# Optimization experiments

Hardware: AMD Instinct MI355X
Metric: run time of the kernel (lower is better)

Reference implementation:

```python
import jax, jax.numpy as jnp
import numpy as np

H = 16
D_MODEL = 1024
D_K = D_MODEL // H
B, S = 4, 2048


def setup_inputs() -> dict:
    key = jax.random.key(0)
    ks = jax.random.split(key, 12)
    scale = 1.0 / np.sqrt(D_MODEL)
    inp = {
        "q": jax.random.normal(ks[0], (B, S, D_MODEL), dtype=jnp.float32),
        "k": jax.random.normal(ks[1], (B, S, D_MODEL), dtype=jnp.float32),
        "v": jax.random.normal(ks[2], (B, S, D_MODEL), dtype=jnp.float32),
        # torch nn.Linear weights: shape (out, in), y = x @ W.T + b
        "Wq": jax.random.uniform(ks[3], (D_MODEL, D_MODEL), minval=-scale, maxval=scale),
        "bq": jax.random.uniform(ks[4], (D_MODEL,), minval=-scale, maxval=scale),
        "Wk": jax.random.uniform(ks[5], (D_MODEL, D_MODEL), minval=-scale, maxval=scale),
        "bk": jax.random.uniform(ks[6], (D_MODEL,), minval=-scale, maxval=scale),
        "Wv": jax.random.uniform(ks[7], (D_MODEL, D_MODEL), minval=-scale, maxval=scale),
        "bv": jax.random.uniform(ks[8], (D_MODEL,), minval=-scale, maxval=scale),
        "Wo": jax.random.uniform(ks[9], (D_MODEL, D_MODEL), minval=-scale, maxval=scale),
        "bo": jax.random.uniform(ks[10], (D_MODEL,), minval=-scale, maxval=scale),
        "ln_g": jnp.ones((D_MODEL,), dtype=jnp.float32),
        "ln_b": jnp.zeros((D_MODEL,), dtype=jnp.float32),
    }
    return inp


def _layernorm(x, g, b, eps=1e-5):
    mu = jnp.mean(x, axis=-1, keepdims=True)
    var = jnp.var(x, axis=-1, keepdims=True)
    return (x - mu) * jax.lax.rsqrt(var + eps) * g + b


def reference(q, k, v, Wq, bq, Wk, bk, Wv, bv, Wo, bo, ln_g, ln_b):
    nb = q.shape[0]
    # projections, split heads -> (B, H, S, d_k)
    def proj(x, W, b):
        y = x @ W.T + b
        return y.reshape(nb, -1, H, D_K).transpose(0, 2, 1, 3)

    Q = proj(q, Wq, bq)
    K = proj(k, Wk, bk)
    V = proj(v, Wv, bv)

    scores = jnp.einsum("bhqd,bhkd->bhqk", Q, K) / jnp.sqrt(jnp.float32(D_K))
    p_attn = jax.nn.softmax(scores, axis=-1)
    x = jnp.einsum("bhqk,bhkd->bhqd", p_attn, V)
    x = x.transpose(0, 2, 1, 3).reshape(nb, -1, H * D_K)
    out = _layernorm(x @ Wo.T + bo + q, ln_g, ln_b)
    return out
```

## Files before the change

### kernel.cpp

```cpp
#include <hip/hip_runtime.h>

#define DM 1024
#define NH 16
#define DK 64
#define SEQ 2048
#define BATCH 4
#define M_TOT (BATCH * SEQ)

typedef short s16x8 __attribute__((ext_vector_type(8)));
typedef float f32x4 __attribute__((ext_vector_type(4)));
typedef unsigned int u32x4 __attribute__((ext_vector_type(4)));
typedef unsigned int u32x2 __attribute__((ext_vector_type(2)));

#define MFMA16(a, b, c) __builtin_amdgcn_mfma_f32_16x16x32_bf16((a), (b), (c), 0, 0, 0)

#define QSCALE 0.1803368801111244f

__device__ __forceinline__ float bf2f(unsigned short u) {
    return __uint_as_float(((unsigned int)u) << 16);
}
__device__ __forceinline__ unsigned short f2bf(float f) {
    unsigned int u = __float_as_uint(f);
    u += 0x7FFFu + ((u >> 16) & 1u);
    return (unsigned short)(u >> 16);
}
__device__ __forceinline__ unsigned int pack_bf2(unsigned int lo, unsigned int hi) {
    return ((lo + 0x8000u) >> 16) | ((hi + 0x8000u) & 0xFFFF0000u);
}
__device__ __forceinline__ unsigned int pack_bf2_trunc(float lo, float hi) {
    return __builtin_amdgcn_perm(__float_as_uint(hi), __float_as_uint(lo), 0x07060302u);
}
__device__ __forceinline__ s16x8 load_cvt8(const float* p) {
    u32x4 x0 = *reinterpret_cast<const u32x4*>(p);
    u32x4 x1 = *reinterpret_cast<const u32x4*>(p + 4);
    union { s16x8 v; unsigned int u[4]; } r;
    r.u[0] = pack_bf2(x0[0], x0[1]);
    r.u[1] = pack_bf2(x0[2], x0[3]);
    r.u[2] = pack_bf2(x1[0], x1[1]);
    r.u[3] = pack_bf2(x1[2], x1[3]);
    return r.v;
}

__device__ __forceinline__ void ld_lds16(const unsigned short* g, unsigned short* lds_base) {
    __builtin_amdgcn_global_load_lds(
        (const __attribute__((address_space(1))) unsigned int*)g,
        (__attribute__((address_space(3))) unsigned int*)lds_base,
        16, 0, 0);
}

__global__ __launch_bounds__(256) void cvt_bf16_kernel(
    const float* __restrict__ src, unsigned short* __restrict__ dst, int n)
{
    const int i = (blockIdx.x * 256 + threadIdx.x) * 8;
    if (i >= n) return;
    *reinterpret_cast<s16x8*>(dst + i) = load_cvt8(src + i);
}

__global__ __launch_bounds__(256) void cvt3_kernel(
    const float* __restrict__ s0, const float* __restrict__ s1,
    const float* __restrict__ s2, unsigned short* __restrict__ dst)
{
    const float* src = blockIdx.z == 0 ? s0 : blockIdx.z == 1 ? s1 : s2;
    const long off = (long)blockIdx.z * ((long)M_TOT * DM);
    const int i = (blockIdx.x * 256 + threadIdx.x) * 8;
    *reinterpret_cast<s16x8*>(dst + off + i) = load_cvt8(src + i);
}

__global__ __launch_bounds__(256) void cvt_w_kernel(
    const float* __restrict__ w0, const float* __restrict__ w1,
    const float* __restrict__ w2, const float* __restrict__ w3,
    unsigned short* __restrict__ dst)
{
    const float* src = blockIdx.y == 0 ? w0 : blockIdx.y == 1 ? w1
                     : blockIdx.y == 2 ? w2 : w3;
    const long off = (long)blockIdx.y * ((long)DM * DM);
    const int i = (blockIdx.x * 256 + threadIdx.x) * 8;
    *reinterpret_cast<s16x8*>(dst + off + i) = load_cvt8(src + i);
}

__device__ __forceinline__ void gemm_body(
    const unsigned short* __restrict__ Ab,
    const unsigned short* __restrict__ Wb,
    const float* __restrict__ bias,
    unsigned short* __restrict__ Y,
    const int mode, const float scale)
{
    const int tid  = threadIdx.x;
    const int lane = tid & 63;
    const int wave = tid >> 6;
    const int c16  = lane & 15;
    const int quad = lane >> 4;
    const int m0 = blockIdx.x * 128;
    const int n0 = blockIdx.y * 128;
    const int wm = (wave >> 1) * 64;
    const int wn = (wave & 1) * 64;

    __shared__ __align__(16) unsigned short As[128 * 32];
    __shared__ __align__(16) unsigned short Bs[128 * 32];

    f32x4 acc[4][4];
    #pragma unroll
    for (int tm = 0; tm < 4; ++tm)
        #pragma unroll
        for (int tn = 0; tn < 4; ++tn) acc[tm][tn] = (f32x4){0.f, 0.f, 0.f, 0.f};

    int srow[2], sch[2];
    #pragma unroll
    for (int c = 0; c < 2; ++c) {
        const int s = c * 256 + wave * 64 + lane;
        srow[c] = s >> 2;
        sch[c]  = s & 3;
    }

    for (int k0 = 0; k0 < DM; k0 += 32) {
        #pragma unroll
        for (int c = 0; c < 2; ++c) {
            unsigned short* abase = As + (c * 256 + wave * 64) * 8;
            unsigned short* bbase = Bs + (c * 256 + wave * 64) * 8;
            ld_lds16(Ab + (long)(m0 + srow[c]) * DM + k0 + sch[c] * 8, abase);
            ld_lds16(Wb + (long)(n0 + srow[c]) * DM + k0 + sch[c] * 8, bbase);
        }
        __syncthreads();

        s16x8 a[4], b[4];
        #pragma unroll
        for (int tm = 0; tm < 4; ++tm)
            a[tm] = *reinterpret_cast<const s16x8*>(As + (wm + tm * 16 + c16) * 32 + quad * 8);
        #pragma unroll
        for (int tn = 0; tn < 4; ++tn)
            b[tn] = *reinterpret_cast<const s16x8*>(Bs + (wn + tn * 16 + c16) * 32 + quad * 8);
        #pragma unroll
        for (int tm = 0; tm < 4; ++tm)
            #pragma unroll
            for (int tn = 0; tn < 4; ++tn)
                acc[tm][tn] = MFMA16(a[tm], b[tn], acc[tm][tn]);
        __syncthreads();
    }

    #pragma unroll
    for (int tn = 0; tn < 4; ++tn) {
        const int col = n0 + wn + tn * 16 + c16;
        const float bv = bias[col];
        const int h = col >> 6, d = col & 63;
        #pragma unroll
        for (int tm = 0; tm < 4; ++tm) {
            #pragma unroll
            for (int r = 0; r < 4; ++r) {
                const int m = m0 + wm + tm * 16 + quad * 4 + r;
                const int b_ = m >> 11;
                const int s  = m & 2047;
                const float v = (acc[tm][tn][r] + bv) * scale;
                long idx;
                if (mode == 0)      idx = (((long)(b_ * NH + h) * SEQ + s) * DK) + d;
                else if (mode == 1) idx = (((long)(b_ * NH + h) * DK + d) * SEQ) + s;
                else                idx = (long)m * DM + col;
                Y[idx] = f2bf(v);
            }
        }
    }
}

__global__ __launch_bounds__(256) void gemm_kernel(
    const unsigned short* __restrict__ Ab,
    const unsigned short* __restrict__ Wb,
    const float* __restrict__ bias,
    unsigned short* __restrict__ Y,
    const int mode, const float scale)
{
    gemm_body(Ab, Wb, bias, Y, mode, scale);
}

__global__ __launch_bounds__(256) void gemm3_kernel(
    const unsigned short* __restrict__ A3,
    const unsigned short* __restrict__ W3,
    const float* __restrict__ bq, const float* __restrict__ bk,
    const float* __restrict__ bv,
    unsigned short* __restrict__ Y3)
{
    const int z = blockIdx.z;
    const long NE = (long)M_TOT * DM;
    const long WEl = (long)DM * DM;
    const unsigned short* Ab = A3 + (long)z * NE;
    const unsigned short* Wb = W3 + (long)z * WEl;
    const float* bias = z == 0 ? bq : z == 1 ? bk : bv;
    unsigned short* Y = Y3 + (long)z * NE;
    const int mode = (z == 2) ? 1 : 0;
    const float scale = (z == 0) ? QSCALE : 1.0f;
    gemm_body(Ab, Wb, bias, Y, mode, scale);
}

__global__ __launch_bounds__(256, 4) void attn_kernel(
    const unsigned short* __restrict__ Qh,
    const unsigned short* __restrict__ Kh,
    const unsigned short* __restrict__ Vt,
    unsigned short* __restrict__ Xo)
{
    const int lane = threadIdx.x & 63;
    const int wave = threadIdx.x >> 6;
    const int c16  = lane & 15;
    const int quad = lane >> 4;
    const int bh = blockIdx.x;
    const int b_ = bh >> 4, h = bh & 15;
    const int m0 = blockIdx.y * 128 + wave * 32;

    __shared__ __align__(16) unsigned short Ks[2 * 64 * 64];
    __shared__ __align__(16) unsigned short Vs[2 * 64 * 64];

    const unsigned short* Kbh = Kh + (long)bh * SEQ * DK;
    const unsigned short* Vbh = Vt + (long)bh * DK * SEQ;

    s16x8 bQ[2][2];
    #pragma unroll
    for (int qt = 0; qt < 2; ++qt) {
        const unsigned short* qb = Qh + ((long)bh * SEQ + m0 + qt * 16 + c16) * DK + quad * 8;
        bQ[qt][0] = *reinterpret_cast<const s16x8*>(qb);
        bQ[qt][1] = *reinterpret_cast<const s16x8*>(qb + 32);
    }

    union { s16x8 v; unsigned int u[4]; } onesu;
    onesu.u[0] = 0x3F803F80u; onesu.u[1] = 0x3F803F80u;
    onesu.u[2] = 0x3F803F80u; onesu.u[3] = 0x3F803F80u;
    const s16x8 onesA = onesu.v;

    f32x4 o[2][4];
    f32x4 lacc[2];
    #pragma unroll
    for (int qt = 0; qt < 2; ++qt) {
        #pragma unroll
        for (int c = 0; c < 4; ++c) o[qt][c] = (f32x4){0.f, 0.f, 0.f, 0.f};
        lacc[qt] = (f32x4){0.f, 0.f, 0.f, 0.f};
    }

    int st_n[4], st_x[4], st_isK[4];
    #pragma unroll
    for (int j = 0; j < 4; ++j) {
        const int c = wave * 4 + j;
        const int s = (c & 7) * 64 + lane;
        st_isK[j] = (c < 8);
        st_n[j] = s >> 3;
        st_x[j] = (s & 7) ^ (st_n[j] & 7);
    }

    auto stage = [&](int buf, int n0) {
        #pragma unroll
        for (int j = 0; j < 4; ++j) {
            const int c = wave * 4 + j;
            if (st_isK[j])
                ld_lds16(Kbh + (n0 + st_n[j]) * DK + st_x[j] * 8,
                         &Ks[buf * 4096 + (c & 7) * 512]);
            else
                ld_lds16(Vbh + (long)st_n[j] * SEQ + n0 + st_x[j] * 8,
                         &Vs[buf * 4096 + (c & 7) * 512]);
        }
    };

    stage(0, 0);
    __syncthreads();

    for (int it = 0; it < SEQ / 64; ++it) {
        const int cur = it & 1;
        if (it + 1 < SEQ / 64) stage(cur ^ 1, (it + 1) * 64);

        const unsigned short* Kb = Ks + cur * 4096;
        const unsigned short* Vb = Vs + cur * 4096;

        f32x4 st[2][4];
        __builtin_amdgcn_s_setprio(1);
        #pragma unroll
        for (int t = 0; t < 4; ++t) {
            const int n = t * 16 + c16;
            const int sw = n & 7;
            s16x8 a0 = *reinterpret_cast<const s16x8*>(&Kb[n * 64 + ((quad ^ sw) * 8)]);
            s16x8 a1 = *reinterpret_cast<const s16x8*>(&Kb[n * 64 + (((quad + 4) ^ sw) * 8)]);
            #pragma unroll
            for (int qt = 0; qt < 2; ++qt) {
                f32x4 s = (f32x4){0.f, 0.f, 0.f, 0.f};
                s = MFMA16(a0, bQ[qt][0], s);
                s = MFMA16(a1, bQ[qt][1], s);
                st[qt][t] = s;
            }
        }
        __builtin_amdgcn_s_setprio(0);

        s16x8 bP[2][2];
        #pragma unroll
        for (int qt = 0; qt < 2; ++qt) {
            #pragma unroll
            for (int t = 0; t < 4; ++t)
                #pragma unroll
                for (int r = 0; r < 4; ++r)
                    st[qt][t][r] = exp2f(st[qt][t][r]);

            uint2 w[4];
            #pragma unroll
            for (int t = 0; t < 4; ++t) {
                w[t].x = pack_bf2_trunc(st[qt][t][0], st[qt][t][1]);
                w[t].y = pack_bf2_trunc(st[qt][t][2], st[qt][t][3]);
            }
            #pragma unroll
            for (int hh = 0; hh < 2; ++hh) {
                u32x2 s0 = __builtin_amdgcn_permlane32_swap(w[2 * hh].x, w[2 * hh + 1].x, false, false);
                u32x2 s1 = __builtin_amdgcn_permlane32_swap(w[2 * hh].y, w[2 * hh + 1].y, false, false);
                u32x2 t0 = __builtin_amdgcn_permlane16_swap(s0[0], s0[1], false, false);
                u32x2 t1 = __builtin_amdgcn_permlane16_swap(s1[0], s1[1], false, false);
                union { s16x8 v; unsigned int u[4]; } f;
                f.u[0] = t0[0];
                f.u[1] = t1[0];
                f.u[2] = t0[1];
                f.u[3] = t1[1];
                bP[qt][hh] = f.v;
            }
        }

        __builtin_amdgcn_s_setprio(1);
        #pragma unroll
        for (int qt = 0; qt < 2; ++qt) {
            lacc[qt] = MFMA16(onesA, bP[qt][0], lacc[qt]);
            lacc[qt] = MFMA16(onesA, bP[qt][1], lacc[qt]);
        }
        #pragma unroll
        for (int cc = 0; cc < 4; ++cc) {
            const int d = cc * 16 + c16;
            const int sw = d & 7;
            s16x8 a0 = *reinterpret_cast<const s16x8*>(&Vb[d * 64 + ((quad ^ sw) * 8)]);
            s16x8 a1 = *reinterpret_cast<const s16x8*>(&Vb[d * 64 + (((quad + 4) ^ sw) * 8)]);
            #pragma unroll
            for (int qt = 0; qt < 2; ++qt) {
                o[qt][cc] = MFMA16(a0, bP[qt][0], o[qt][cc]);
                o[qt][cc] = MFMA16(a1, bP[qt][1], o[qt][cc]);
            }
        }
        __builtin_amdgcn_s_setprio(0);
        __syncthreads();
    }

    #pragma unroll
    for (int qt = 0; qt < 2; ++qt) {
        const float inv = 1.f / lacc[qt][0];
        unsigned short* orow = Xo + ((long)b_ * SEQ + m0 + qt * 16 + c16) * DM + h * DK;
        #pragma unroll
        for (int c = 0; c < 4; ++c) {
            uint2 w;
            w.x = pack_bf2(__float_as_uint(o[qt][c][0] * inv), __float_as_uint(o[qt][c][1] * inv));
            w.y = pack_bf2(__float_as_uint(o[qt][c][2] * inv), __float_as_uint(o[qt][c][3] * inv));
            *reinterpret_cast<uint2*>(orow + c * 16 + quad * 4) = w;
        }
    }
}

__global__ __launch_bounds__(256) void ln_kernel(
    const unsigned short* __restrict__ Xlin,
    const float* __restrict__ qres,
    const float* __restrict__ g,
    const float* __restrict__ bb,
    float* __restrict__ out)
{
    const int row = blockIdx.x;
    const int tid = threadIdx.x;
    const int c0 = tid * 4;
    const int lane = tid & 63, wave = tid >> 6;

    __shared__ float ssum[4], ssq[4];

    uint2 xb = *reinterpret_cast<const uint2*>(Xlin + (long)row * DM + c0);
    float4 qv = *reinterpret_cast<const float4*>(qres + (long)row * DM + c0);
    float v[4];
    v[0] = bf2f((unsigned short)(xb.x & 0xFFFF)) + qv.x;
    v[1] = bf2f((unsigned short)(xb.x >> 16))    + qv.y;
    v[2] = bf2f((unsigned short)(xb.y & 0xFFFF)) + qv.z;
    v[3] = bf2f((unsigned short)(xb.y >> 16))    + qv.w;

    float s = v[0] + v[1] + v[2] + v[3];
    float q2 = v[0]*v[0] + v[1]*v[1] + v[2]*v[2] + v[3]*v[3];
    #pragma unroll
    for (int d = 1; d < 64; d <<= 1) {
        s  += __shfl_xor(s, d, 64);
        q2 += __shfl_xor(q2, d, 64);
    }
    if (lane == 0) { ssum[wave] = s; ssq[wave] = q2; }
    __syncthreads();
    const float ts = ssum[0] + ssum[1] + ssum[2] + ssum[3];
    const float tq = ssq[0] + ssq[1] + ssq[2] + ssq[3];
    const float mu = ts * (1.f / 1024.f);
    const float var = tq * (1.f / 1024.f) - mu * mu;
    const float rstd = rsqrtf(var + 1e-5f);

    float4 gv = *reinterpret_cast<const float4*>(g + c0);
    float4 bv = *reinterpret_cast<const float4*>(bb + c0);
    float4 o;
    o.x = (v[0] - mu) * rstd * gv.x + bv.x;
    o.y = (v[1] - mu) * rstd * gv.y + bv.y;
    o.z = (v[2] - mu) * rstd * gv.z + bv.z;
    o.w = (v[3] - mu) * rstd * gv.w + bv.w;
    *reinterpret_cast<float4*>(out + (long)row * DM + c0) = o;
}

extern "C" void kernel_launch(void* const* d_in, const int* in_sizes, int n_in,
                              void* d_out, int out_size, void* d_ws, size_t ws_size,
                              hipStream_t stream) {
    const float* q   = (const float*)d_in[0];
    const float* k   = (const float*)d_in[1];
    const float* v   = (const float*)d_in[2];
    const float* Wq  = (const float*)d_in[3];
    const float* bq  = (const float*)d_in[4];
    const float* Wk  = (const float*)d_in[5];
    const float* bk  = (const float*)d_in[6];
    const float* Wv  = (const float*)d_in[7];
    const float* bvv = (const float*)d_in[8];
    const float* Wo  = (const float*)d_in[9];
    const float* bo  = (const float*)d_in[10];
    const float* lng = (const float*)d_in[11];
    const float* lnb = (const float*)d_in[12];

    unsigned short* ws = (unsigned short*)d_ws;
    const long WE = (long)DM * DM;
    const long NE = (long)M_TOT * DM;

    dim3 blk(256);
    const int cvtW = (int)(WE / 2048);
    const int cvtX = (int)(NE / 2048);
    dim3 ggemm(M_TOT / 128, DM / 128);

    const size_t need_batched = (size_t)(4 * WE + 6 * NE) * sizeof(unsigned short);

    if (ws_size >= need_batched) {
        unsigned short* Wqb = ws;
        unsigned short* Wob = Wqb + 3 * WE;
        unsigned short* A3  = Wqb + 4 * WE;
        unsigned short* O3  = A3 + 3 * NE;
        unsigned short* Xo   = A3;
        unsigned short* Xlin = A3 + NE;

        cvt_w_kernel<<<dim3(cvtW, 4), blk, 0, stream>>>(Wq, Wk, Wv, Wo, Wqb);
        cvt3_kernel<<<dim3(cvtX, 1, 3), blk, 0, stream>>>(q, k, v, A3);
        gemm3_kernel<<<dim3(M_TOT / 128, DM / 128, 3), blk, 0, stream>>>(
            A3, Wqb, bq, bk, bvv, O3);
        attn_kernel<<<dim3(BATCH * NH, SEQ / 128), blk, 0, stream>>>(
            O3, O3 + NE, O3 + 2 * NE, Xo);
        gemm_kernel<<<ggemm, blk, 0, stream>>>(Xo, Wob, bo, Xlin, 2, 1.0f);
        ln_kernel<<<dim3(M_TOT), blk, 0, stream>>>(Xlin, q, lng, lnb, (float*)d_out);
    } else {
        unsigned short* Wqb = ws;
        unsigned short* Wkb = Wqb + WE;
        unsigned short* Wvb = Wkb + WE;
        unsigned short* Wob = Wvb + WE;
        unsigned short* U1  = Wob + WE;
        unsigned short* U2  = U1 + NE;
        unsigned short* U3  = U2 + NE;
        unsigned short* U4  = U3 + NE;

        cvt_w_kernel<<<dim3(cvtW, 4), blk, 0, stream>>>(Wq, Wk, Wv, Wo, Wqb);
        cvt_bf16_kernel<<<cvtX, blk, 0, stream>>>(q, U1, (int)NE);
        gemm_kernel<<<ggemm, blk, 0, stream>>>(U1, Wqb, bq, U2, 0, QSCALE);
        cvt_bf16_kernel<<<cvtX, blk, 0, stream>>>(k, U1, (int)NE);
        gemm_kernel<<<ggemm, blk, 0, stream>>>(U1, Wkb, bk, U3, 0, 1.0f);
        cvt_bf16_kernel<<<cvtX, blk, 0, stream>>>(v, U1, (int)NE);
        gemm_kernel<<<ggemm, blk, 0, stream>>>(U1, Wvb, bvv, U4, 1, 1.0f);
        attn_kernel<<<dim3(BATCH * NH, SEQ / 128), blk, 0, stream>>>(U2, U3, U4, U1);
        gemm_kernel<<<ggemm, blk, 0, stream>>>(U1, Wob, bo, U2, 2, 1.0f);
        ln_kernel<<<dim3(M_TOT), blk, 0, stream>>>(U2, q, lng, lnb, (float*)d_out);
    }
}
```

Baseline: 397.0 us.

## Permute K rows at staging to drop permlane swaps; add XCD-aware GEMM tile mapping

```diff
diff --git a/kernel.cpp b/kernel.cpp
--- a/kernel.cpp
+++ b/kernel.cpp
@@ -10,7 +10,6 @@
 typedef short s16x8 __attribute__((ext_vector_type(8)));
 typedef float f32x4 __attribute__((ext_vector_type(4)));
 typedef unsigned int u32x4 __attribute__((ext_vector_type(4)));
-typedef unsigned int u32x2 __attribute__((ext_vector_type(2)));
 
 #define MFMA16(a, b, c) __builtin_amdgcn_mfma_f32_16x16x32_bf16((a), (b), (c), 0, 0, 0)
 
@@ -90,8 +89,15 @@
     const int wave = tid >> 6;
     const int c16  = lane & 15;
     const int quad = lane >> 4;
-    const int m0 = blockIdx.x * 128;
-    const int n0 = blockIdx.y * 128;
+
+    const int flat  = blockIdx.y * gridDim.x + blockIdx.x;
+    const int xcd   = flat & 7;
+    const int w     = flat >> 3;
+    const int m_blk = xcd * 8 + (w & 7);
+    const int n_blk = w >> 3;
+    const int m0 = m_blk * 128;
+    const int n0 = n_blk * 128;
+
     const int wm = (wave >> 1) * 64;
     const int wn = (wave & 1) * 64;
 
@@ -231,14 +237,17 @@
         lacc[qt] = (f32x4){0.f, 0.f, 0.f, 0.f};
     }
 
-    int st_n[4], st_x[4], st_isK[4];
+    int st_src[4], st_x[4], st_isK[4];
     #pragma unroll
     for (int j = 0; j < 4; ++j) {
         const int c = wave * 4 + j;
         const int s = (c & 7) * 64 + lane;
+        const int m = s >> 3;
         st_isK[j] = (c < 8);
-        st_n[j] = s >> 3;
-        st_x[j] = (s & 7) ^ (st_n[j] & 7);
+        st_x[j] = (s & 7) ^ (m & 7);
+        st_src[j] = st_isK[j]
+            ? ( (((m >> 4) & 1) << 5) | (((m >> 2) & 3) << 3) | (((m >> 5) & 1) << 2) | (m & 3) )
+            : m;
     }
 
     auto stage = [&](int buf, int n0) {
@@ -246,10 +255,10 @@
         for (int j = 0; j < 4; ++j) {
             const int c = wave * 4 + j;
             if (st_isK[j])
-                ld_lds16(Kbh + (n0 + st_n[j]) * DK + st_x[j] * 8,
+                ld_lds16(Kbh + (n0 + st_src[j]) * DK + st_x[j] * 8,
                          &Ks[buf * 4096 + (c & 7) * 512]);
             else
-                ld_lds16(Vbh + (long)st_n[j] * SEQ + n0 + st_x[j] * 8,
+                ld_lds16(Vbh + (long)st_src[j] * SEQ + n0 + st_x[j] * 8,
                          &Vs[buf * 4096 + (c & 7) * 512]);
         }
     };
@@ -291,23 +300,13 @@
                 for (int r = 0; r < 4; ++r)
                     st[qt][t][r] = exp2f(st[qt][t][r]);
 
-            uint2 w[4];
-            #pragma unroll
-            for (int t = 0; t < 4; ++t) {
-                w[t].x = pack_bf2_trunc(st[qt][t][0], st[qt][t][1]);
-                w[t].y = pack_bf2_trunc(st[qt][t][2], st[qt][t][3]);
-            }
             #pragma unroll
             for (int hh = 0; hh < 2; ++hh) {
-                u32x2 s0 = __builtin_amdgcn_permlane32_swap(w[2 * hh].x, w[2 * hh + 1].x, false, false);
-                u32x2 s1 = __builtin_amdgcn_permlane32_swap(w[2 * hh].y, w[2 * hh + 1].y, false, false);
-                u32x2 t0 = __builtin_amdgcn_permlane16_swap(s0[0], s0[1], false, false);
-                u32x2 t1 = __builtin_amdgcn_permlane16_swap(s1[0], s1[1], false, false);
                 union { s16x8 v; unsigned int u[4]; } f;
-                f.u[0] = t0[0];
-                f.u[1] = t1[0];
-                f.u[2] = t0[1];
-                f.u[3] = t1[1];
+                f.u[0] = pack_bf2_trunc(st[qt][hh][0],     st[qt][hh][1]);
+                f.u[1] = pack_bf2_trunc(st[qt][hh][2],     st[qt][hh][3]);
+                f.u[2] = pack_bf2_trunc(st[qt][hh + 2][0], st[qt][hh + 2][1]);
+                f.u[3] = pack_bf2_trunc(st[qt][hh + 2][2], st[qt][hh + 2][3]);
                 bP[qt][hh] = f.v;
             }
         }
```

New measurement: 382.5 us. -3.7%, faster.
